# Optimization experiments

Hardware: AMD Instinct MI355X
Metric: run time of the kernel (lower is better)

Reference implementation:

```python
import jax, jax.numpy as jnp
from jax import lax
import numpy as np

TAG_NAMES = ["O", "B-MAT", "I-MAT", "B-PRO", "I-PRO", "B-APL", "I-APL", "B-SMT", "I-SMT", "B-CMT", "I-CMT", "B-DSC", "I-DSC"]
IMP = -100.0


def _init_crf_params(key):
    # torchcrf initializes uniform(-0.1, 0.1); CRF_NEW then clamps invalid
    # BIO transitions to -100 per define_invalid_crf_transitions/init_crf_transitions.
    K = len(TAG_NAMES)
    k1, k2, k3 = jax.random.split(key, 3)
    start = np.array(jax.random.uniform(k1, (K,), minval=-0.1, maxval=0.1), dtype=np.float32)
    end = np.array(jax.random.uniform(k2, (K,), minval=-0.1, maxval=0.1), dtype=np.float32)
    trans = np.array(jax.random.uniform(k3, (K, K), minval=-0.1, maxval=0.1), dtype=np.float32)
    pref = [t[0] for t in TAG_NAMES]
    ent = [t.split('-')[1] if '-' in t else '' for t in TAG_NAMES]
    for i in range(K):
        if pref[i] in ('B', 'I'):  # invalid begin/end for BIO
            start[i] = IMP
            end[i] = IMP
    for i in range(K):
        for j in range(K):
            # invalid_transitions_position: O -> I  (B->P, I->P are empty sets)
            if pref[i] == 'O' and pref[j] == 'I':
                trans[i, j] = IMP
            # invalid_transitions_tags: B->I, I->I across different entity types
            if pref[i] in ('B', 'I') and pref[j] == 'I' and ent[i] != ent[j]:
                trans[i, j] = IMP
    return jnp.asarray(start), jnp.asarray(end), jnp.asarray(trans)


def setup_inputs() -> dict:
    key = jax.random.key(0)
    k_em, k_tag, k_p = jax.random.split(key, 3)
    B, T, K = 4096, 512, len(TAG_NAMES)
    emissions = jax.random.normal(k_em, (B, T, K), dtype=jnp.float32)
    tags = jax.random.randint(k_tag, (B, T), 0, K, dtype=jnp.int64)
    mask = jnp.ones((B, T), dtype=bool)
    start_transitions, end_transitions, transitions = _init_crf_params(k_p)
    return {"emissions": emissions, "tags": tags, "mask": mask,
            "start_transitions": start_transitions,
            "end_transitions": end_transitions,
            "transitions": transitions}


def reference(emissions, tags, mask, start_transitions, end_transitions, transitions):
    # torchcrf CRF.forward with batch_first=True, reduction='sum':
    # returns sum over batch of log p(tags | emissions).
    B, T, K = emissions.shape
    maskf = mask.astype(emissions.dtype)

    # ---- numerator: score of the given tag path ----
    emit = jnp.take_along_axis(emissions, tags[..., None], axis=2)[..., 0]  # [B,T]
    trans = transitions[tags[:, :-1], tags[:, 1:]]                           # [B,T-1]
    num = start_transitions[tags[:, 0]] + emit[:, 0]
    num = num + jnp.sum((trans + emit[:, 1:]) * maskf[:, 1:], axis=1)
    seq_ends = jnp.sum(mask.astype(jnp.int32), axis=1) - 1                   # [B]
    last_tags = tags[jnp.arange(B), seq_ends]
    num = num + end_transitions[last_tags]

    # ---- denominator: log partition via forward-algorithm scan over time ----
    em_t = jnp.swapaxes(emissions, 0, 1)   # [T,B,K]
    mask_t = jnp.swapaxes(mask, 0, 1)      # [T,B]
    score0 = start_transitions + em_t[0]   # [B,K]

    def step(score, xs):
        em, m = xs  # em: [B,K], m: [B]
        # broadcast: [B,K_from,1] + [K_from,K_to] + [B,1,K_to]
        nxt = jax.nn.logsumexp(score[:, :, None] + transitions[None] + em[:, None, :], axis=1)
        return jnp.where(m[:, None], nxt, score), None

    score, _ = lax.scan(step, score0, (em_t[1:], mask_t[1:]))
    denom = jax.nn.logsumexp(score + end_transitions, axis=1)  # [B]

    return jnp.sum(num - denom)
```

## Files before the change

kernel.cpp:

```cpp
#include <hip/hip_runtime.h>


typedef float  f4  __attribute__((ext_vector_type(4)));
typedef float  f4u __attribute__((ext_vector_type(4), aligned(4)));
typedef short  s4  __attribute__((ext_vector_type(4)));
typedef int    i2  __attribute__((ext_vector_type(2)));

#define FENCE do { __builtin_amdgcn_sched_barrier(0); \
                   asm volatile("" ::: "memory"); } while (0)

__device__ __forceinline__ unsigned pack_bf16(float x, float y) {
  return __builtin_amdgcn_perm(__float_as_uint(y) + 0x8000u,
                               __float_as_uint(x) + 0x8000u, 0x07060302u);
}

__global__ void __launch_bounds__(128, 1)
crf_main(const float* __restrict__ em,
         const int*   __restrict__ tags,
         const float* __restrict__ startT,
         const float* __restrict__ endT,
         const float* __restrict__ trans,
         float* __restrict__ partial)
{
  __shared__ float ldsT[256];
  __shared__ float ldsS[16], ldsE[16];
  __shared__ float pFa[256];
  __shared__ float lsF[16], numF[16], resB[16];
  __shared__ int   tag255[16];

  const int tid = threadIdx.x;
  for (int i = tid; i < 169; i += 128) {
    const int r_ = i / 13, c_ = i - r_ * 13;
    ldsT[r_ * 16 + c_] = trans[i];
  }
  if (tid < 13) ldsS[tid] = startT[tid];
  if (tid >= 16 && tid < 29) ldsE[tid - 16] = endT[tid - 16];
  __syncthreads();

  const int lane = tid & 63;
  const int n    = lane & 15;
  const int q    = lane >> 4;
  const bool is_fwd = (tid < 64);
  const int seq  = blockIdx.x * 16 + n;
  const int loadBase = (q < 3) ? 4 * q : 9;
  const int lo       = (q < 3) ? 4 * q : 12;
  const unsigned span = (q < 3) ? 3u : 0u;
  const float* emP = em + (size_t)seq * 6656 + loadBase;
  const int*   tgP = tags + (size_t)seq * 512;

  s4 afrag;
  {
    float av[4];
#pragma unroll
    for (int i = 0; i < 4; ++i) {
      const int kk = 4 * q + i;
      av[i] = (kk < 13 && n < 13)
            ? __expf(is_fwd ? ldsT[kk * 16 + n] : ldsT[n * 16 + kk]) : 0.0f;
    }
    i2 ai = { (int)pack_bf16(av[0], av[1]), (int)pack_bf16(av[2], av[3]) };
    afrag = __builtin_bit_cast(s4, ai);
  }

  f4 D;
#pragma unroll
  for (int r = 0; r < 4; ++r) {
    const int m = 4 * q + r;
    D[r] = (m < 13) ? __expf(is_fwd ? ldsS[m] : ldsE[m]) : 0.0f;
  }

  float logscale = 0.0f, em_acc = 0.0f, trans_acc = 0.0f;
  float sDs0 = 0, sDs1 = 0, sDs2 = 0, sDs3 = 0;
  float start_t0 = 0.0f;
  int tg_hi = 0, tg_lo = 0, tg511 = 0;
  f4 eA[16], eB[16];
  int4 tA[4], tB[4];

#define TGV(TB, k) ((((k) & 3) == 0) ? TB[(k) >> 2].x : (((k) & 3) == 1) ? TB[(k) >> 2].y \
                  : (((k) & 3) == 2) ? TB[(k) >> 2].z : TB[(k) >> 2].w)

#define LOADC(EB, TB, TC) do {                                          \
    const int tc_ = (TC);                                               \
    _Pragma("unroll")                                                   \
    for (int k_ = 0; k_ < 16; ++k_)                                     \
      EB[k_] = *(const f4u*)(emP + (size_t)(tc_ + k_) * 13);            \
    _Pragma("unroll")                                                   \
    for (int g_ = 0; g_ < 4; ++g_)                                      \
      TB[g_] = *(const int4*)(tgP + tc_ + 4 * g_);                      \
  } while (0)

#define RENORM4() do {                                                  \
    float cm_ = fmaxf(fmaxf(Ds0, Ds1), fmaxf(Ds2, Ds3));                \
    cm_ = fmaxf(cm_, __shfl_xor(cm_, 16, 64));                          \
    cm_ = fmaxf(cm_, __shfl_xor(cm_, 32, 64));                          \
    const float rc_ = __builtin_amdgcn_rcpf(cm_);                       \
    Ds0 *= rc_; Ds1 *= rc_; Ds2 *= rc_; Ds3 *= rc_;                     \
    logscale += __logf(cm_);                                            \
  } while (0)

#define CORE(EM4, RN, TGVv) do {                                        \
    const float e0 = __expf((q == 3) ? (EM4).w : (EM4).x);              \
    const float e1 = __expf((EM4).y);                                   \
    const float e2 = __expf((EM4).z);                                   \
    const float e3 = __expf((EM4).w);                                   \
    Ds0 = D[0] * e0; Ds1 = D[1] * e1; Ds2 = D[2] * e2; Ds3 = D[3] * e3; \
    if (RN) RENORM4();                                                  \
    {                                                                   \
      const unsigned ur_ = (unsigned)((TGVv) - lo);                     \
      const int rr_ = (TGVv) - loadBase;                                \
      const float s01_ = (rr_ & 1) ? (EM4).y : (EM4).x;                 \
      const float s23_ = (rr_ & 1) ? (EM4).w : (EM4).z;                 \
      const float sv_  = (rr_ & 2) ? s23_ : s01_;                       \
      em_acc += (ur_ <= span) ? sv_ : 0.0f;                             \
    }                                                                   \
    {                                                                   \
      i2 bi_ = { (int)pack_bf16(Ds0, Ds1), (int)pack_bf16(Ds2, Ds3) };  \
      s4 bf_ = __builtin_bit_cast(s4, bi_);                             \
      D = __builtin_amdgcn_mfma_f32_16x16x16bf16_1k(                    \
              afrag, bf_, (f4){0.f, 0.f, 0.f, 0.f}, 0, 0, 0);           \
    }                                                                   \
  } while (0)

#define PROCF(EB, TB, FIRST, LAST) do {                                 \
    _Pragma("unroll")                                                   \
    for (int k = 0; k < 16; ++k) {                                      \
      const int tgv = TGV(TB, k);                                       \
      if (FIRST && k == 0) start_t0 = ldsS[tgv];                        \
      else {                                                            \
        const int pv = (k == 0) ? tg_hi : TGV(TB, k - 1);               \
        trans_acc += ldsT[pv * 16 + tgv];                               \
      }                                                                 \
      const f4 em4 = EB[k];                                             \
      float Ds0, Ds1, Ds2, Ds3;                                         \
      CORE(em4, (k == 7 || k == 15), tgv);                              \
      if (LAST && k == 15) { sDs0 = Ds0; sDs1 = Ds1; sDs2 = Ds2; sDs3 = Ds3; } \
    }                                                                   \
    tg_hi = TGV(TB, 15);                                                \
  } while (0)

#define PROCB(EB, TB, FIRST) do {                                       \
    if (FIRST) tg511 = TGV(TB, 15);                                     \
    else       trans_acc += ldsT[TGV(TB, 15) * 16 + tg_lo];             \
    _Pragma("unroll")                                                   \
    for (int kk = 0; kk < 16; ++kk) {                                   \
      const int k = 15 - kk;                                            \
      const int tgv = TGV(TB, k);                                       \
      if (k > 0) trans_acc += ldsT[TGV(TB, k - 1) * 16 + tgv];          \
      const f4 em4 = EB[k];                                             \
      float Ds0, Ds1, Ds2, Ds3;                                         \
      CORE(em4, (k == 8 || k == 0), tgv);                               \
    }                                                                   \
    tg_lo = TGV(TB, 0);                                                 \
  } while (0)

  if (is_fwd) {
    LOADC(eA, tA, 0); LOADC(eB, tB, 16); FENCE;
    PROCF(eA, tA, true, false);
    for (int it = 0; it < 7; ++it) {
      LOADC(eA, tA, 32 * it + 32); FENCE;
      PROCF(eB, tB, false, false);
      LOADC(eB, tB, 32 * it + 48); FENCE;
      PROCF(eA, tA, false, false);
    }
    FENCE;
    PROCF(eB, tB, false, true);
    float emr = em_acc + __shfl_xor(em_acc, 16, 64);
    emr += __shfl_xor(emr, 32, 64);
    if (q == 0) {
      lsF[n]    = logscale;
      numF[n]   = start_t0 + emr + trans_acc;
      tag255[n] = tg_hi;
    }
    *(f4*)&pFa[n * 16 + 4 * q] = (f4){sDs0, sDs1, sDs2, sDs3};
  } else {
    LOADC(eA, tA, 496); LOADC(eB, tB, 480); FENCE;
    PROCB(eA, tA, true);
    for (int it = 0; it < 7; ++it) {
      LOADC(eA, tA, 464 - 32 * it); FENCE;
      PROCB(eB, tB, false);
      LOADC(eB, tB, 448 - 32 * it); FENCE;
      PROCB(eA, tA, false);
    }
    FENCE;
    PROCB(eB, tB, false);
  }

  __syncthreads();

  if (!is_fwd) {
    const f4 al = *(const f4*)&pFa[n * 16 + 4 * q];
    float z = al[0] * D[0] + al[1] * D[1] + al[2] * D[2] + al[3] * D[3];
    z += __shfl_xor(z, 16, 64);
    z += __shfl_xor(z, 32, 64);
    float emr = em_acc + __shfl_xor(em_acc, 16, 64);
    emr += __shfl_xor(emr, 32, 64);
    const float denom = lsF[n] + logscale + __logf(z);
    const float num   = numF[n] + emr + trans_acc
                      + ldsT[tag255[n] * 16 + tg_lo]
                      + ldsE[tg511];
    if (q == 0) resB[n] = num - denom;
  }
  __syncthreads();
  if (tid == 0) {
    float s = 0.0f;
#pragma unroll
    for (int i = 0; i < 16; ++i) s += resB[i];
    partial[blockIdx.x] = s;
  }

#undef TGV
#undef LOADC
#undef RENORM4
#undef CORE
#undef PROCF
#undef PROCB
}

__global__ void __launch_bounds__(256)
crf_reduce(const float* __restrict__ part, float* __restrict__ out, int n)
{
  float v = 0.0f;
  for (int i = threadIdx.x; i < n; i += 256) v += part[i];
#pragma unroll
  for (int off = 32; off > 0; off >>= 1) v += __shfl_down(v, off);
  __shared__ float w[4];
  if ((threadIdx.x & 63) == 0) w[threadIdx.x >> 6] = v;
  __syncthreads();
  if (threadIdx.x == 0) out[0] = (w[0] + w[1]) + (w[2] + w[3]);
}

extern "C" void kernel_launch(void* const* d_in, const int* in_sizes, int n_in,
                              void* d_out, int out_size, void* d_ws, size_t ws_size,
                              hipStream_t stream) {
  const float* em   = (const float*)d_in[0];
  const int*   tags = (const int*)d_in[1];
  const float* st   = (const float*)d_in[3];
  const float* en   = (const float*)d_in[4];
  const float* tr   = (const float*)d_in[5];
  float* part = (float*)d_ws;

  crf_main<<<256, 128, 0, stream>>>(em, tags, st, en, tr, part);
  crf_reduce<<<1, 256, 0, stream>>>(part, (float*)d_out, 256);
}
```

Before: 186.7 us.

## Stage emissions and tags through LDS with async global_load_lds triple buffering

```diff
diff --git a/kernel.cpp b/kernel.cpp
--- a/kernel.cpp
+++ b/kernel.cpp
@@ -2,17 +2,23 @@
 
 
 typedef float  f4  __attribute__((ext_vector_type(4)));
-typedef float  f4u __attribute__((ext_vector_type(4), aligned(4)));
 typedef short  s4  __attribute__((ext_vector_type(4)));
 typedef int    i2  __attribute__((ext_vector_type(2)));
-
-#define FENCE do { __builtin_amdgcn_sched_barrier(0); \
-                   asm volatile("" ::: "memory"); } while (0)
 
 __device__ __forceinline__ unsigned pack_bf16(float x, float y) {
   return __builtin_amdgcn_perm(__float_as_uint(y) + 0x8000u,
                                __float_as_uint(x) + 0x8000u, 0x07060302u);
 }
+
+__device__ __forceinline__ void gll16(const void* g, void* l) {
+  __builtin_amdgcn_global_load_lds(
+      (const __attribute__((address_space(1))) void*)g,
+      (__attribute__((address_space(3))) void*)l, 16, 0, 0);
+}
+
+#define VMWAIT(N) do { asm volatile("s_waitcnt vmcnt(" #N ")" ::: "memory"); \
+                       __builtin_amdgcn_sched_barrier(0); } while (0)
+#define SB0() __builtin_amdgcn_sched_barrier(0)
 
 __global__ void __launch_bounds__(128, 1)
 crf_main(const float* __restrict__ em,
@@ -22,6 +28,8 @@
          const float* __restrict__ trans,
          float* __restrict__ partial)
 {
+  __shared__ __align__(16) float emST[2][3][4096];
+  __shared__ __align__(16) int   tagST[2][3][256];
   __shared__ float ldsT[256];
   __shared__ float ldsS[16], ldsE[16];
   __shared__ float pFa[256];
@@ -41,12 +49,14 @@
   const int n    = lane & 15;
   const int q    = lane >> 4;
   const bool is_fwd = (tid < 64);
-  const int seq  = blockIdx.x * 16 + n;
+  const int  w   = is_fwd ? 0 : 1;
+  const int  seq = blockIdx.x * 16 + n;
   const int loadBase = (q < 3) ? 4 * q : 9;
   const int lo       = (q < 3) ? 4 * q : 12;
   const unsigned span = (q < 3) ? 3u : 0u;
-  const float* emP = em + (size_t)seq * 6656 + loadBase;
-  const int*   tgP = tags + (size_t)seq * 512;
+  const float* emL = em   + (size_t)seq * 6656 + loadBase;
+  const int*   tgL = tags + (size_t)seq * 512 + 4 * q;
+  const int   lofs = lane * 4;
 
   s4 afrag;
   {
@@ -72,20 +82,24 @@
   float sDs0 = 0, sDs1 = 0, sDs2 = 0, sDs3 = 0;
   float start_t0 = 0.0f;
   int tg_hi = 0, tg_lo = 0, tg511 = 0;
-  f4 eA[16], eB[16];
-  int4 tA[4], tB[4];
-
-#define TGV(TB, k) ((((k) & 3) == 0) ? TB[(k) >> 2].x : (((k) & 3) == 1) ? TB[(k) >> 2].y \
-                  : (((k) & 3) == 2) ? TB[(k) >> 2].z : TB[(k) >> 2].w)
-
-#define LOADC(EB, TB, TC) do {                                          \
-    const int tc_ = (TC);                                               \
-    _Pragma("unroll")                                                   \
-    for (int k_ = 0; k_ < 16; ++k_)                                     \
-      EB[k_] = *(const f4u*)(emP + (size_t)(tc_ + k_) * 13);            \
-    _Pragma("unroll")                                                   \
-    for (int g_ = 0; g_ < 4; ++g_)                                      \
-      TB[g_] = *(const int4*)(tgP + tc_ + 4 * g_);                      \
+  int4 tG[4];
+
+#define TGV(k) ((((k) & 3) == 0) ? tG[(k) >> 2].x : (((k) & 3) == 1) ? tG[(k) >> 2].y \
+              : (((k) & 3) == 2) ? tG[(k) >> 2].z : tG[(k) >> 2].w)
+
+#define STAGE(SL, TC) do {                                               \
+    float* eb_ = &emST[w][SL][0];                                        \
+    const float* gp_ = emL + (size_t)(TC) * 13;                          \
+    _Pragma("unroll")                                                    \
+    for (int k_ = 0; k_ < 16; ++k_)                                      \
+      gll16(gp_ + (size_t)k_ * 13, eb_ + k_ * 256);                      \
+    gll16(tgL + (TC), &tagST[w][SL][0]);                                 \
+  } while (0)
+
+#define LDTAGS(SL) do {                                                  \
+    _Pragma("unroll")                                                    \
+    for (int g_ = 0; g_ < 4; ++g_)                                       \
+      tG[g_] = *(const int4*)&tagST[w][SL][(g_ * 16 + n) * 4];           \
   } while (0)
 
 #define RENORM4() do {                                                  \
@@ -120,49 +134,50 @@
     }                                                                   \
   } while (0)
 
-#define PROCF(EB, TB, FIRST, LAST) do {                                 \
+#define PROCF(SL, FIRST, LAST) do {                                     \
     _Pragma("unroll")                                                   \
     for (int k = 0; k < 16; ++k) {                                      \
-      const int tgv = TGV(TB, k);                                       \
+      const int tgv = TGV(k);                                           \
       if (FIRST && k == 0) start_t0 = ldsS[tgv];                        \
       else {                                                            \
-        const int pv = (k == 0) ? tg_hi : TGV(TB, k - 1);               \
+        const int pv = (k == 0) ? tg_hi : TGV(k - 1);                   \
         trans_acc += ldsT[pv * 16 + tgv];                               \
       }                                                                 \
-      const f4 em4 = EB[k];                                             \
+      const f4 em4 = *(const f4*)&emST[w][SL][k * 256 + lofs];          \
       float Ds0, Ds1, Ds2, Ds3;                                         \
       CORE(em4, (k == 7 || k == 15), tgv);                              \
       if (LAST && k == 15) { sDs0 = Ds0; sDs1 = Ds1; sDs2 = Ds2; sDs3 = Ds3; } \
     }                                                                   \
-    tg_hi = TGV(TB, 15);                                                \
-  } while (0)
-
-#define PROCB(EB, TB, FIRST) do {                                       \
-    if (FIRST) tg511 = TGV(TB, 15);                                     \
-    else       trans_acc += ldsT[TGV(TB, 15) * 16 + tg_lo];             \
+    tg_hi = TGV(15);                                                    \
+  } while (0)
+
+#define PROCB(SL, FIRST) do {                                           \
+    if (FIRST) tg511 = TGV(15);                                         \
+    else       trans_acc += ldsT[TGV(15) * 16 + tg_lo];                 \
     _Pragma("unroll")                                                   \
     for (int kk = 0; kk < 16; ++kk) {                                   \
       const int k = 15 - kk;                                            \
-      const int tgv = TGV(TB, k);                                       \
-      if (k > 0) trans_acc += ldsT[TGV(TB, k - 1) * 16 + tgv];          \
-      const f4 em4 = EB[k];                                             \
+      const int tgv = TGV(k);                                           \
+      if (k > 0) trans_acc += ldsT[TGV(k - 1) * 16 + tgv];              \
+      const f4 em4 = *(const f4*)&emST[w][SL][k * 256 + lofs];          \
       float Ds0, Ds1, Ds2, Ds3;                                         \
       CORE(em4, (k == 8 || k == 0), tgv);                               \
     }                                                                   \
-    tg_lo = TGV(TB, 0);                                                 \
+    tg_lo = TGV(0);                                                     \
   } while (0)
 
   if (is_fwd) {
-    LOADC(eA, tA, 0); LOADC(eB, tB, 16); FENCE;
-    PROCF(eA, tA, true, false);
-    for (int it = 0; it < 7; ++it) {
-      LOADC(eA, tA, 32 * it + 32); FENCE;
-      PROCF(eB, tB, false, false);
-      LOADC(eB, tB, 32 * it + 48); FENCE;
-      PROCF(eA, tA, false, false);
-    }
-    FENCE;
-    PROCF(eB, tB, false, true);
+    STAGE(0, 0); STAGE(1, 16); STAGE(2, 32);
+    VMWAIT(34); LDTAGS(0); PROCF(0, true, false); SB0(); STAGE(0, 48);
+#pragma unroll 1
+    for (int c = 1; c <= 10; c += 3) {
+      VMWAIT(34); LDTAGS(1); PROCF(1, false, false); SB0(); STAGE(1, 16 * c + 48);
+      VMWAIT(34); LDTAGS(2); PROCF(2, false, false); SB0(); STAGE(2, 16 * c + 64);
+      VMWAIT(34); LDTAGS(0); PROCF(0, false, false); SB0(); STAGE(0, 16 * c + 80);
+    }
+    VMWAIT(34); LDTAGS(1); PROCF(1, false, false);
+    VMWAIT(17); LDTAGS(2); PROCF(2, false, false);
+    VMWAIT(0);  LDTAGS(0); PROCF(0, false, true);
     float emr = em_acc + __shfl_xor(em_acc, 16, 64);
     emr += __shfl_xor(emr, 32, 64);
     if (q == 0) {
@@ -172,16 +187,17 @@
     }
     *(f4*)&pFa[n * 16 + 4 * q] = (f4){sDs0, sDs1, sDs2, sDs3};
   } else {
-    LOADC(eA, tA, 496); LOADC(eB, tB, 480); FENCE;
-    PROCB(eA, tA, true);
-    for (int it = 0; it < 7; ++it) {
-      LOADC(eA, tA, 464 - 32 * it); FENCE;
-      PROCB(eB, tB, false);
-      LOADC(eB, tB, 448 - 32 * it); FENCE;
-      PROCB(eA, tA, false);
-    }
-    FENCE;
-    PROCB(eB, tB, false);
+    STAGE(0, 496); STAGE(1, 480); STAGE(2, 464);
+    VMWAIT(34); LDTAGS(0); PROCB(0, true); SB0(); STAGE(0, 448);
+#pragma unroll 1
+    for (int c = 1; c <= 10; c += 3) {
+      VMWAIT(34); LDTAGS(1); PROCB(1, false); SB0(); STAGE(1, 448 - 16 * c);
+      VMWAIT(34); LDTAGS(2); PROCB(2, false); SB0(); STAGE(2, 432 - 16 * c);
+      VMWAIT(34); LDTAGS(0); PROCB(0, false); SB0(); STAGE(0, 416 - 16 * c);
+    }
+    VMWAIT(34); LDTAGS(1); PROCB(1, false);
+    VMWAIT(17); LDTAGS(2); PROCB(2, false);
+    VMWAIT(0);  LDTAGS(0); PROCB(0, false);
   }
 
   __syncthreads();
@@ -208,7 +224,8 @@
   }
 
 #undef TGV
-#undef LOADC
+#undef STAGE
+#undef LDTAGS
 #undef RENORM4
 #undef CORE
 #undef PROCF
```

Result: slower. 194.3 us (+4.1%).
